# Kernel optimization log

Hardware: AMD Instinct MI355X
Metric: run time of the kernel (lower is better)

## Reference

```python
import jax, jax.numpy as jnp
import numpy as np

B, N, DIN = 16, 1024, 256
HEADS, OUT_DIM = 4, 256
F = OUT_DIM // HEADS  # per-head feature dim
NEG_SLOPE = 0.2
MASK_VAL = -1e9


def setup_inputs() -> dict:
    key = jax.random.key(0)
    k1, k2, k3, k4, k5, k6 = jax.random.split(key, 6)
    x = jax.random.normal(k1, (B, N, DIN), dtype=jnp.float32)
    adj = jax.random.uniform(k2, (B, N, N), dtype=jnp.float32)  # >0.5 -> edge
    # GATConv learned params (Glorot-ish scale)
    W = jax.random.normal(k3, (DIN, HEADS, F), dtype=jnp.float32) * (1.0 / np.sqrt(DIN))
    a_src = jax.random.normal(k4, (HEADS, F), dtype=jnp.float32) * (1.0 / np.sqrt(F))
    a_dst = jax.random.normal(k5, (HEADS, F), dtype=jnp.float32) * (1.0 / np.sqrt(F))
    bias = jax.random.normal(k6, (OUT_DIM,), dtype=jnp.float32) * 0.01
    return {"x": x, "adj": adj, "W": W, "a_src": a_src, "a_dst": a_dst, "bias": bias}


def reference(x, adj, W, a_src, a_dst, bias):
    # GAT over a dense adjacency mask: mathematically identical to
    # per-sample tf.where edge extraction + edge-list GATConv (softmax over
    # j with adj[b,i,j] > 0.5), but fully vectorized over the batch.
    b, n, _ = x.shape
    h = jnp.einsum('bnd,dhf->bnhf', x, W)                  # [B,N,H,F]
    e_src = jnp.einsum('bnhf,hf->bhn', h, a_src)           # source logits
    e_dst = jnp.einsum('bnhf,hf->bhn', h, a_dst)           # target logits
    # e[b,h,i,j]: edge j -> i
    e = e_dst[:, :, :, None] + e_src[:, :, None, :]        # [B,H,N,N]
    e = jax.nn.leaky_relu(e, NEG_SLOPE)
    mask = (adj > 0.5)[:, None, :, :]                      # [B,1,N,N]
    e = jnp.where(mask, e, MASK_VAL)
    attn = jax.nn.softmax(e, axis=-1)                      # softmax over sources j
    out = jnp.einsum('bhij,bjhf->bihf', attn, h)           # aggregate messages
    out = out.reshape(b, n, HEADS * F) + bias              # concat heads + bias
    return out
```

## Files before the change

kernel.cpp:

```cpp
#include <hip/hip_runtime.h>

#define B_    16
#define N_    1024
#define DIN_  256
#define H_    4
#define F_    64
#define COUT_ 256
#define NEG_  0.2f
#define LOG2E_ 1.4426950408889634f

typedef __bf16 bf16x8 __attribute__((ext_vector_type(8)));
typedef float  f32x4  __attribute__((ext_vector_type(4)));
typedef unsigned short u16x8 __attribute__((ext_vector_type(8)));
typedef unsigned short u16x4 __attribute__((ext_vector_type(4)));
typedef unsigned int   u32x4 __attribute__((ext_vector_type(4)));

__device__ __forceinline__ unsigned short f2bf(float f) {
    unsigned u = __builtin_bit_cast(unsigned, f);
    u += 0x7fffu + ((u >> 16) & 1u);
    return (unsigned short)(u >> 16);
}

__global__ __launch_bounds__(256) void prep_kernel(
    const float* __restrict__ W, unsigned short* __restrict__ Wtp) {
    const int c = blockIdx.x, k = threadIdx.x;
    const int w = c >> 6, ft = (c >> 4) & 3, l15 = c & 15;
    const int it = k >> 5, q = (k >> 3) & 3, jj = k & 7;
    const int ln = q * 16 + l15;
    Wtp[((((w * 8 + it) * 4 + ft) * 64) + ln) * 8 + jj] = f2bf(W[k * COUT_ + c]);
}

__global__ __launch_bounds__(256, 4) void stage_kernel(
    const float* __restrict__ adj, const float* __restrict__ x,
    const unsigned short* __restrict__ Wtp, const float* __restrict__ a_src,
    const float* __restrict__ a_dst, unsigned int* __restrict__ mask,
    unsigned short* __restrict__ hp, float* __restrict__ e_src,
    float* __restrict__ e_dst) {
    if (blockIdx.x < 2048) {
        const int b  = blockIdx.x >> 7;
        const int jc = (blockIdx.x >> 2) & 31;
        const int r  = (blockIdx.x & 3) * 256 + threadIdx.x;
        const float* arow = adj + (size_t)(b * N_ + r) * N_ + jc * 32;
        unsigned u = 0;
#pragma unroll
        for (int k = 0; k < 8; k++) {
            f32x4 v = *(const f32x4*)(arow + k * 4);
#pragma unroll
            for (int i2 = 0; i2 < 4; i2++)
                u |= (v[i2] > 0.5f) ? (1u << (k * 4 + i2)) : 0u;
        }
        mask[(b * 32 + jc) * N_ + r] = u;
    } else {
        const int blk = blockIdx.x - 2048;
        const int b   = blk & 15;
        const int it0 = (blk >> 4) * 16;
        const int w   = threadIdx.x >> 6;
        const int ln  = threadIdx.x & 63;
        const int l15 = ln & 15;
        const int q   = ln >> 4;

        const float* xrow = x + (size_t)(b * N_ + it0 + l15) * DIN_;

        f32x4 xv[8];
#pragma unroll
        for (int it = 0; it < 4; it++) {
            xv[2 * it]     = *(const f32x4*)(xrow + it * 32 + q * 8);
            xv[2 * it + 1] = *(const f32x4*)(xrow + it * 32 + q * 8 + 4);
        }
        f32x4 xw[8];
#pragma unroll
        for (int it = 0; it < 4; it++) {
            xw[2 * it]     = *(const f32x4*)(xrow + (it + 4) * 32 + q * 8);
            xw[2 * it + 1] = *(const f32x4*)(xrow + (it + 4) * 32 + q * 8 + 4);
        }
        bf16x8 af[4];
#pragma unroll
        for (int it = 0; it < 4; it++) {
            u16x8 u;
#pragma unroll
            for (int jj = 0; jj < 4; jj++) {
                u[jj]     = f2bf(xv[2 * it][jj]);
                u[jj + 4] = f2bf(xv[2 * it + 1][jj]);
            }
            af[it] = __builtin_bit_cast(bf16x8, u);
        }

        f32x4 acc[4];
#pragma unroll
        for (int ft = 0; ft < 4; ft++) acc[ft] = (f32x4)0.0f;

        const unsigned short* wb = Wtp + (w * 8) * 4 * 64 * 8 + ln * 8;
#pragma unroll
        for (int it = 0; it < 4; it++)
#pragma unroll
            for (int ft = 0; ft < 4; ft++) {
                bf16x8 bf = *((const bf16x8*)(wb + (it * 4 + ft) * 512));
                acc[ft] = __builtin_amdgcn_mfma_f32_16x16x32_bf16(af[it], bf, acc[ft], 0, 0, 0);
            }
        bf16x8 ag[4];
#pragma unroll
        for (int it = 0; it < 4; it++) {
            u16x8 u;
#pragma unroll
            for (int jj = 0; jj < 4; jj++) {
                u[jj]     = f2bf(xw[2 * it][jj]);
                u[jj + 4] = f2bf(xw[2 * it + 1][jj]);
            }
            ag[it] = __builtin_bit_cast(bf16x8, u);
        }
#pragma unroll
        for (int it = 0; it < 4; it++)
#pragma unroll
            for (int ft = 0; ft < 4; ft++) {
                bf16x8 bf = *((const bf16x8*)(wb + ((it + 4) * 4 + ft) * 512));
                acc[ft] = __builtin_amdgcn_mfma_f32_16x16x32_bf16(ag[it], bf, acc[ft], 0, 0, 0);
            }

        const int jg = it0 >> 5;
        const int q2 = 2 * ((it0 >> 4) & 1) + (q >> 1);
#pragma unroll
        for (int ft = 0; ft < 4; ft++) {
            u16x4 hb;
#pragma unroll
            for (int r = 0; r < 4; r++) hb[r] = f2bf(acc[ft][r]);
            const size_t addr =
                (size_t)((((b * H_ + w) * 32 + jg) * 4 + ft) * 64 + q2 * 16 + l15) * 8 + (q & 1) * 4;
            *((u16x4*)(hp + addr)) = hb;
        }

        float as_v[4], ad_v[4];
#pragma unroll
        for (int ft = 0; ft < 4; ft++) {
            as_v[ft] = a_src[w * F_ + ft * 16 + l15];
            ad_v[ft] = a_dst[w * F_ + ft * 16 + l15];
        }
        float ps[4], pd[4];
#pragma unroll
        for (int r = 0; r < 4; r++) {
            ps[r] = 0.0f; pd[r] = 0.0f;
#pragma unroll
            for (int ft = 0; ft < 4; ft++) {
                ps[r] += acc[ft][r] * as_v[ft];
                pd[r] += acc[ft][r] * ad_v[ft];
            }
        }
#pragma unroll
        for (int off = 1; off <= 8; off <<= 1)
#pragma unroll
            for (int r = 0; r < 4; r++) {
                ps[r] += __shfl_xor(ps[r], off);
                pd[r] += __shfl_xor(pd[r], off);
            }
        float vs = (l15 == 0) ? ps[0] : (l15 == 1) ? ps[1] : (l15 == 2) ? ps[2] : ps[3];
        float vd = (l15 == 0) ? pd[0] : (l15 == 1) ? pd[1] : (l15 == 2) ? pd[2] : pd[3];
        if (l15 < 4) {
            const int i = it0 + q * 4 + l15;
            e_src[(b * H_ + w) * N_ + i] = vs * LOG2E_;
            e_dst[(b * H_ + w) * N_ + i] = vd * LOG2E_;
        }
    }
}

__global__ __launch_bounds__(512, 4) void gat_attn_kernel(
    const unsigned int* __restrict__ mask, const unsigned short* __restrict__ hp,
    const float* __restrict__ e_src, const float* __restrict__ e_dst,
    const float* __restrict__ bias, float* __restrict__ out) {
    const int b   = blockIdx.x & 15;
    const int it0 = (blockIdx.x >> 4) * 32;
    const int w8  = threadIdx.x >> 6;
    const int h   = w8 & 3;
    const int jh  = w8 >> 2;
    const int ln  = threadIdx.x & 63;
    const int l15 = ln & 15;
    const int q   = ln >> 4;

    __shared__ float lds[H_][2][5][64][4];

    float edv[2];
    edv[0] = e_dst[(b * H_ + h) * N_ + it0 + l15];
    edv[1] = e_dst[(b * H_ + h) * N_ + it0 + 16 + l15];

    const float* es_base           = e_src + (b * H_ + h) * N_;
    const unsigned short* hp_base  = hp + (size_t)((b * H_ + h) * 32) * 2048 + ln * 8;
    const unsigned int* mk0        = mask + b * 32 * N_ + it0;

    f32x4 acc[2][4];
    f32x4 accs[2];
#pragma unroll
    for (int mt = 0; mt < 2; mt++) {
#pragma unroll
        for (int ft = 0; ft < 4; ft++) acc[mt][ft] = (f32x4)0.0f;
        accs[mt] = (f32x4)0.0f;
    }

    u16x8 ones_u;
#pragma unroll
    for (int jj = 0; jj < 8; jj++) ones_u[jj] = 0x3F80;
    const bf16x8 ones = __builtin_bit_cast(bf16x8, ones_u);

    for (int jg = jh * 16; jg < jh * 16 + 16; jg++) {
        const int jb = jg * 32 + q * 8;
        const unsigned short* hf = hp_base + jg * 2048;
        bf16x8 bfr0 = *((const bf16x8*)(hf + 0 * 512));
        bf16x8 bfr1 = *((const bf16x8*)(hf + 1 * 512));
        bf16x8 bfr2 = *((const bf16x8*)(hf + 2 * 512));
        bf16x8 bfr3 = *((const bf16x8*)(hf + 3 * 512));
        f32x4 e0 = *(const f32x4*)(es_base + jb);
        f32x4 e1 = *(const f32x4*)(es_base + jb + 4);
        const unsigned m0 = mk0[jg * N_ + l15];
        const unsigned m1 = mk0[jg * N_ + 16 + l15];
        const unsigned mq0 = (m0 >> (q * 8)) & 0xffu;
        const unsigned mq1 = (m1 >> (q * 8)) & 0xffu;

        float es8[8] = {e0[0], e0[1], e0[2], e0[3], e1[0], e1[1], e1[2], e1[3]};

        bf16x8 afr[2];
#pragma unroll
        for (int mt = 0; mt < 2; mt++) {
            const unsigned mq = mt ? mq1 : mq0;
            u32x4 up;
#pragma unroll
            for (int p2 = 0; p2 < 4; p2++) {
                float t0 = edv[mt] + es8[2 * p2];
                float t1 = edv[mt] + es8[2 * p2 + 1];
                t0 = fmaxf(t0, NEG_ * t0);
                t1 = fmaxf(t1, NEG_ * t1);
                float p0 = __builtin_amdgcn_exp2f(t0);
                float p1 = __builtin_amdgcn_exp2f(t1);
                p0 = ((mq >> (2 * p2)) & 1u) ? p0 : 0.0f;
                p1 = ((mq >> (2 * p2 + 1)) & 1u) ? p1 : 0.0f;
                up[p2] = __builtin_amdgcn_perm(__builtin_bit_cast(unsigned, p1),
                                               __builtin_bit_cast(unsigned, p0),
                                               0x07060302u);
            }
            afr[mt] = __builtin_bit_cast(bf16x8, up);
        }
#pragma unroll
        for (int mt = 0; mt < 2; mt++) {
            acc[mt][0] = __builtin_amdgcn_mfma_f32_16x16x32_bf16(afr[mt], bfr0, acc[mt][0], 0, 0, 0);
            acc[mt][1] = __builtin_amdgcn_mfma_f32_16x16x32_bf16(afr[mt], bfr1, acc[mt][1], 0, 0, 0);
            acc[mt][2] = __builtin_amdgcn_mfma_f32_16x16x32_bf16(afr[mt], bfr2, acc[mt][2], 0, 0, 0);
            acc[mt][3] = __builtin_amdgcn_mfma_f32_16x16x32_bf16(afr[mt], bfr3, acc[mt][3], 0, 0, 0);
            accs[mt]   = __builtin_amdgcn_mfma_f32_16x16x32_bf16(afr[mt], ones, accs[mt], 0, 0, 0);
        }
    }

    if (jh == 1) {
#pragma unroll
        for (int mt = 0; mt < 2; mt++) {
#pragma unroll
            for (int ft = 0; ft < 4; ft++)
                *(f32x4*)&lds[h][mt][ft][ln][0] = acc[mt][ft];
            *(f32x4*)&lds[h][mt][4][ln][0] = accs[mt];
        }
    }
    __syncthreads();
    if (jh == 0) {
#pragma unroll
        for (int mt = 0; mt < 2; mt++) {
#pragma unroll
            for (int ft = 0; ft < 4; ft++)
                acc[mt][ft] += *(const f32x4*)&lds[h][mt][ft][ln][0];
            accs[mt] += *(const f32x4*)&lds[h][mt][4][ln][0];
        }
        float bias_v[4];
#pragma unroll
        for (int ft = 0; ft < 4; ft++) bias_v[ft] = bias[h * F_ + ft * 16 + l15];
#pragma unroll
        for (int mt = 0; mt < 2; mt++) {
            f32x4 rinv;
#pragma unroll
            for (int r = 0; r < 4; r++) rinv[r] = 1.0f / accs[mt][r];
#pragma unroll
            for (int ft = 0; ft < 4; ft++)
#pragma unroll
                for (int r = 0; r < 4; r++) {
                    const int i = it0 + mt * 16 + q * 4 + r;
                    const int c = h * F_ + ft * 16 + l15;
                    out[(size_t)(b * N_ + i) * COUT_ + c] = acc[mt][ft][r] * rinv[r] + bias_v[ft];
                }
        }
    }
}

extern "C" void kernel_launch(void* const* d_in, const int* in_sizes, int n_in,
                              void* d_out, int out_size, void* d_ws, size_t ws_size,
                              hipStream_t stream) {
    const float* x     = (const float*)d_in[0];
    const float* adj   = (const float*)d_in[1];
    const float* W     = (const float*)d_in[2];
    const float* a_src = (const float*)d_in[3];
    const float* a_dst = (const float*)d_in[4];
    const float* bias  = (const float*)d_in[5];
    float* out = (float*)d_out;

    char* ws = (char*)d_ws;
    unsigned short* Wtp = (unsigned short*)ws;
    unsigned short* hp  = (unsigned short*)(ws + 131072);
    float* e_src        = (float*)(ws + 131072 + 8388608);
    float* e_dst        = (float*)(ws + 131072 + 8388608 + 262144);
    unsigned int* mask  = (unsigned int*)(ws + 131072 + 8388608 + 524288);

    prep_kernel<<<256, 256, 0, stream>>>(W, Wtp);
    stage_kernel<<<3072, 256, 0, stream>>>(adj, x, Wtp, a_src, a_dst, mask, hp, e_src, e_dst);
    gat_attn_kernel<<<512, 512, 0, stream>>>(mask, hp, e_src, e_dst, bias, out);
}
```

Before: 155.9 us.

## Coalesce adjacency mask build and stage x tile through LDS for projection

The mask-building blocks now assign one wavefront per adjacency row, so each lane reads a contiguous float4 across the row and nibbles are combined with xor-shuffles into 32-bit mask words. This replaces the old scheme where each thread read a strided 128-byte chunk of its own row. The projection blocks now load x rows coalesced, convert them to bf16 into a shared-memory tile, and read MFMA A fragments from LDS. That replaces scattered per-lane global loads held in registers. The cost is more blocks, an extra __syncthreads, LDS use, and mask stores that are scattered across rows.

New measurement: 150.3 us. 1.04x faster.

```diff
diff --git a/kernel.cpp b/kernel.cpp
--- a/kernel.cpp
+++ b/kernel.cpp
@@ -36,54 +36,47 @@
     const float* __restrict__ a_dst, unsigned int* __restrict__ mask,
     unsigned short* __restrict__ hp, float* __restrict__ e_src,
     float* __restrict__ e_dst) {
-    if (blockIdx.x < 2048) {
-        const int b  = blockIdx.x >> 7;
-        const int jc = (blockIdx.x >> 2) & 31;
-        const int r  = (blockIdx.x & 3) * 256 + threadIdx.x;
-        const float* arow = adj + (size_t)(b * N_ + r) * N_ + jc * 32;
-        unsigned u = 0;
-#pragma unroll
-        for (int k = 0; k < 8; k++) {
-            f32x4 v = *(const f32x4*)(arow + k * 4);
-#pragma unroll
-            for (int i2 = 0; i2 < 4; i2++)
-                u |= (v[i2] > 0.5f) ? (1u << (k * 4 + i2)) : 0u;
-        }
-        mask[(b * 32 + jc) * N_ + r] = u;
+    __shared__ unsigned short xs[16][264];
+    const int w  = threadIdx.x >> 6;
+    const int ln = threadIdx.x & 63;
+
+    if (blockIdx.x < 4096) {
+        const int row = blockIdx.x * 4 + w;
+        const int b = row >> 10, i = row & (N_ - 1);
+        const float* ar = adj + (size_t)row * N_ + ln * 4;
+#pragma unroll
+        for (int c = 0; c < 4; c++) {
+            f32x4 v = *(const f32x4*)(ar + c * 256);
+            unsigned nib = 0;
+#pragma unroll
+            for (int e = 0; e < 4; e++)
+                nib |= (v[e] > 0.5f) ? (1u << e) : 0u;
+            unsigned word = nib << ((ln & 7) * 4);
+            word |= __shfl_xor(word, 1);
+            word |= __shfl_xor(word, 2);
+            word |= __shfl_xor(word, 4);
+            if ((ln & 7) == 0) {
+                const int jc = c * 8 + (ln >> 3);
+                mask[(b * 32 + jc) * N_ + i] = word;
+            }
+        }
     } else {
-        const int blk = blockIdx.x - 2048;
+        const int blk = blockIdx.x - 4096;
         const int b   = blk & 15;
         const int it0 = (blk >> 4) * 16;
-        const int w   = threadIdx.x >> 6;
-        const int ln  = threadIdx.x & 63;
         const int l15 = ln & 15;
         const int q   = ln >> 4;
 
-        const float* xrow = x + (size_t)(b * N_ + it0 + l15) * DIN_;
-
-        f32x4 xv[8];
-#pragma unroll
-        for (int it = 0; it < 4; it++) {
-            xv[2 * it]     = *(const f32x4*)(xrow + it * 32 + q * 8);
-            xv[2 * it + 1] = *(const f32x4*)(xrow + it * 32 + q * 8 + 4);
-        }
-        f32x4 xw[8];
-#pragma unroll
-        for (int it = 0; it < 4; it++) {
-            xw[2 * it]     = *(const f32x4*)(xrow + (it + 4) * 32 + q * 8);
-            xw[2 * it + 1] = *(const f32x4*)(xrow + (it + 4) * 32 + q * 8 + 4);
-        }
-        bf16x8 af[4];
-#pragma unroll
-        for (int it = 0; it < 4; it++) {
-            u16x8 u;
-#pragma unroll
-            for (int jj = 0; jj < 4; jj++) {
-                u[jj]     = f2bf(xv[2 * it][jj]);
-                u[jj + 4] = f2bf(xv[2 * it + 1][jj]);
-            }
-            af[it] = __builtin_bit_cast(bf16x8, u);
-        }
+#pragma unroll
+        for (int s = 0; s < 4; s++) {
+            const int row = w * 4 + s;
+            f32x4 xv = *(const f32x4*)(x + (size_t)(b * N_ + it0 + row) * DIN_ + ln * 4);
+            unsigned lo = (unsigned)f2bf(xv[0]) | ((unsigned)f2bf(xv[1]) << 16);
+            unsigned hi = (unsigned)f2bf(xv[2]) | ((unsigned)f2bf(xv[3]) << 16);
+            unsigned long long hb = (unsigned long long)lo | ((unsigned long long)hi << 32);
+            *(unsigned long long*)&xs[row][ln * 4] = hb;
+        }
+        __syncthreads();
 
         f32x4 acc[4];
 #pragma unroll
@@ -91,30 +84,14 @@
 
         const unsigned short* wb = Wtp + (w * 8) * 4 * 64 * 8 + ln * 8;
 #pragma unroll
-        for (int it = 0; it < 4; it++)
+        for (int it = 0; it < 8; it++) {
+            bf16x8 af = *(const bf16x8*)&xs[l15][it * 32 + q * 8];
 #pragma unroll
             for (int ft = 0; ft < 4; ft++) {
                 bf16x8 bf = *((const bf16x8*)(wb + (it * 4 + ft) * 512));
-                acc[ft] = __builtin_amdgcn_mfma_f32_16x16x32_bf16(af[it], bf, acc[ft], 0, 0, 0);
-            }
-        bf16x8 ag[4];
-#pragma unroll
-        for (int it = 0; it < 4; it++) {
-            u16x8 u;
-#pragma unroll
-            for (int jj = 0; jj < 4; jj++) {
-                u[jj]     = f2bf(xw[2 * it][jj]);
-                u[jj + 4] = f2bf(xw[2 * it + 1][jj]);
-            }
-            ag[it] = __builtin_bit_cast(bf16x8, u);
-        }
-#pragma unroll
-        for (int it = 0; it < 4; it++)
-#pragma unroll
-            for (int ft = 0; ft < 4; ft++) {
-                bf16x8 bf = *((const bf16x8*)(wb + ((it + 4) * 4 + ft) * 512));
-                acc[ft] = __builtin_amdgcn_mfma_f32_16x16x32_bf16(ag[it], bf, acc[ft], 0, 0, 0);
-            }
+                acc[ft] = __builtin_amdgcn_mfma_f32_16x16x32_bf16(af, bf, acc[ft], 0, 0, 0);
+            }
+        }
 
         const int jg = it0 >> 5;
         const int q2 = 2 * ((it0 >> 4) & 1) + (q >> 1);
@@ -180,9 +157,9 @@
     edv[0] = e_dst[(b * H_ + h) * N_ + it0 + l15];
     edv[1] = e_dst[(b * H_ + h) * N_ + it0 + 16 + l15];
 
-    const float* es_base           = e_src + (b * H_ + h) * N_;
-    const unsigned short* hp_base  = hp + (size_t)((b * H_ + h) * 32) * 2048 + ln * 8;
-    const unsigned int* mk0        = mask + b * 32 * N_ + it0;
+    const float* es_base          = e_src + (b * H_ + h) * N_;
+    const unsigned short* hp_base = hp + (size_t)((b * H_ + h) * 32) * 2048 + ln * 8;
+    const unsigned int* mk0       = mask + b * 32 * N_ + it0;
 
     f32x4 acc[2][4];
     f32x4 accs[2];
@@ -199,25 +176,22 @@
     const bf16x8 ones = __builtin_bit_cast(bf16x8, ones_u);
 
     for (int jg = jh * 16; jg < jh * 16 + 16; jg++) {
-        const int jb = jg * 32 + q * 8;
         const unsigned short* hf = hp_base + jg * 2048;
         bf16x8 bfr0 = *((const bf16x8*)(hf + 0 * 512));
         bf16x8 bfr1 = *((const bf16x8*)(hf + 1 * 512));
         bf16x8 bfr2 = *((const bf16x8*)(hf + 2 * 512));
         bf16x8 bfr3 = *((const bf16x8*)(hf + 3 * 512));
-        f32x4 e0 = *(const f32x4*)(es_base + jb);
-        f32x4 e1 = *(const f32x4*)(es_base + jb + 4);
+        f32x4 e0 = *(const f32x4*)(es_base + jg * 32 + q * 8);
+        f32x4 e1 = *(const f32x4*)(es_base + jg * 32 + q * 8 + 4);
         const unsigned m0 = mk0[jg * N_ + l15];
         const unsigned m1 = mk0[jg * N_ + 16 + l15];
-        const unsigned mq0 = (m0 >> (q * 8)) & 0xffu;
-        const unsigned mq1 = (m1 >> (q * 8)) & 0xffu;
 
         float es8[8] = {e0[0], e0[1], e0[2], e0[3], e1[0], e1[1], e1[2], e1[3]};
 
         bf16x8 afr[2];
 #pragma unroll
         for (int mt = 0; mt < 2; mt++) {
-            const unsigned mq = mt ? mq1 : mq0;
+            const unsigned mq = ((mt ? m1 : m0) >> (q * 8)) & 0xffu;
             u32x4 up;
 #pragma unroll
             for (int p2 = 0; p2 < 4; p2++) {
@@ -302,6 +276,6 @@
     unsigned int* mask  = (unsigned int*)(ws + 131072 + 8388608 + 524288);
 
     prep_kernel<<<256, 256, 0, stream>>>(W, Wtp);
-    stage_kernel<<<3072, 256, 0, stream>>>(adj, x, Wtp, a_src, a_dst, mask, hp, e_src, e_dst);
+    stage_kernel<<<5120, 256, 0, stream>>>(adj, x, Wtp, a_src, a_dst, mask, hp, e_src, e_dst);
     gat_attn_kernel<<<512, 512, 0, stream>>>(mask, hp, e_src, e_dst, bias, out);
 }
```
